# Performance work log

Measured on AMD Instinct MI355X. Metric: run time of the kernel, lower is better.

Reference implementation:

```python
import jax, jax.numpy as jnp
import numpy as np

N_STEPS = 10
LOG2PI = float(np.log(2.0 * np.pi))
# Dormand-Prince 5(4) tableau; only the 6 stages feeding the 5th-order solution (b7=0)
_C = (0.0, 1/5, 3/10, 4/5, 8/9, 1.0)
_A = ((),
      (1/5,),
      (3/40, 9/40),
      (44/45, -56/15, 32/9),
      (19372/6561, -25360/2187, 64448/6561, -212/729),
      (9017/3168, -355/33, 46732/5247, 49/176, -5103/18656))
_B = (35/384, 0.0, 500/1113, 125/192, -2187/6784, 11/84)


def _mlp(x, t, cond, W1, b1, W2, b2, W3, b3):
    # state_time_derivative_fn: f(t, x; cond) -> dx/dt
    tcol = jnp.full((x.shape[0], 1), t, dtype=x.dtype)
    h = jnp.concatenate([x, tcol, cond], axis=-1)
    h = jnp.tanh(h @ W1 + b1)
    h = jnp.tanh(h @ W2 + b2)
    return h @ W3 + b3


def _flow_log_prob(x, cond, eps, params):
    """FFJORD log_prob: integrate augmented state (x, logdet) from t=1 -> t=0
    with fixed-step DOPRI5; Hutchinson trace eps^T J eps via jvp."""
    B, D = x.shape

    def dyn(xx, t):
        f = lambda u: _mlp(u, t, cond, *params)
        dx, jeps = jax.jvp(f, (xx,), (eps,))
        tr = jnp.sum(jeps * eps, axis=-1)  # [B] Hutchinson trace estimate
        return dx, tr

    dt = -1.0 / N_STEPS  # integrate backward in time (inverse / log_prob pass)

    def step(carry, t0):
        xx, L = carry
        kx, kl = [], []
        for i in range(6):
            xi = xx
            for j in range(i):
                xi = xi + (dt * _A[i][j]) * kx[j]
            dxi, tri = dyn(xi, t0 + _C[i] * dt)
            kx.append(dxi)
            kl.append(tri)
        xx = xx + dt * sum(b * k for b, k in zip(_B, kx))
        L = L + dt * sum(b * k for b, k in zip(_B, kl))
        return (xx, L), None

    ts = 1.0 + dt * jnp.arange(N_STEPS, dtype=x.dtype)
    (z, L), _ = jax.lax.scan(jax.checkpoint(step), (x, jnp.zeros(B, x.dtype)), ts)
    # base distribution: standard multivariate normal
    logpz = -0.5 * jnp.sum(z * z, axis=-1) - 0.5 * D * LOG2PI
    return logpz + L


def setup_inputs() -> dict:
    key = jax.random.key(0)
    B, D, E, C, H = 8192, 504, 45, 1, 512
    ks = jax.random.split(key, 20)
    g = lambda k, shp: jax.random.normal(k, shp, jnp.float32)
    w = lambda k, fi, fo: g(k, (fi, fo)) * (1.0 / np.sqrt(fi))
    inp = {
        'voxel': g(ks[0], (B, D)),
        'energy': g(ks[1], (B, E)),
        'cond': jax.random.uniform(ks[2], (B, C), jnp.float32),
        'eps_v': g(ks[3], (B, D)),
        'eps_e': g(ks[4], (B, E)),
        # voxel-flow MLP: input = [x(D), t(1), energy(E)+cond(C)]
        'W1v': w(ks[5], D + 1 + E + C, H), 'b1v': jnp.zeros((H,), jnp.float32),
        'W2v': w(ks[6], H, H), 'b2v': jnp.zeros((H,), jnp.float32),
        'W3v': w(ks[7], H, D) * 0.1, 'b3v': jnp.zeros((D,), jnp.float32),
        # energy-flow MLP: input = [e(E), t(1), cond(C)]
        'W1e': w(ks[8], E + 1 + C, H), 'b1e': jnp.zeros((H,), jnp.float32),
        'W2e': w(ks[9], H, H), 'b2e': jnp.zeros((H,), jnp.float32),
        'W3e': w(ks[10], H, E) * 0.1, 'b3e': jnp.zeros((E,), jnp.float32),
    }
    return inp


def reference(voxel, energy, cond, eps_v, eps_e,
              W1v, b1v, W2v, b2v, W3v, b3v,
              W1e, b1e, W2e, b2e, W3e, b3e):
    # log_loss: voxel flow conditioned on concat([energies, conditional])
    cond_v = jnp.concatenate([energy, cond], axis=-1)
    lp_v = _flow_log_prob(voxel, cond_v, eps_v, (W1v, b1v, W2v, b2v, W3v, b3v))
    # log_loss_energy: energy flow conditioned on conditional
    lp_e = _flow_log_prob(energy, cond, eps_e, (W1e, b1e, W2e, b2e, W3e, b3e))
    loss_voxel = -jnp.mean(lp_v)
    loss_energy = -jnp.mean(lp_e)
    return loss_voxel + loss_energy
```

## Files before the change

### kernel.cpp

```cpp
#include <hip/hip_runtime.h>
#include <math.h>
#include <stdint.h>

#define LOG2PI 1.8378770664093453f

typedef __attribute__((ext_vector_type(8))) short bf8;
typedef __attribute__((ext_vector_type(4))) float f4;

__device__ __forceinline__ short f2bf(float f) {
    uint32_t u = __float_as_uint(f);
    u += 0x7fffu + ((u >> 16) & 1u);
    return (short)(u >> 16);
}
__device__ __forceinline__ float bf2f(unsigned short u) {
    return __uint_as_float(((uint32_t)u) << 16);
}
__device__ __forceinline__ float tanh_fast(float x) {
    float t = __builtin_amdgcn_exp2f(x * 2.88539008177793f);
    return 1.f - 2.f * __builtin_amdgcn_rcpf(1.f + t);
}
__device__ __forceinline__ bf8 ntl8(const short* p) {
    return *(const bf8*)p;
}
__device__ __forceinline__ void gload16(const void* g, void* l) {
    __builtin_amdgcn_global_load_lds(
        (const __attribute__((address_space(1))) uint32_t*)(uintptr_t)g,
        (__attribute__((address_space(3))) uint32_t*)(uintptr_t)l, 16, 0, 0);
}

struct FA {
    float* Pcurf; short* Pcurb; const short* th1b; const short* vbufp;
    short* Pk; float* xf;
    const short* w2t; const short* w3c;
    const float* b2; const float* b3p; const float* b31; const float* wtp;
    float* L;
};

__global__ __launch_bounds__(512, 2) void stage2_k(
    FA f0, FA f1, int i, float ti,
    float c0, float c1, float c2, float c3, float c4,
    float tcoef, float db0, float db2, float db3, float db4, float db5)
{
    __shared__ char lds[65536];
    const int tid = threadIdx.x, wave = tid >> 6, lane = tid & 63;
    const int lr = lane >> 4, lc = lane & 15;
    const int fl = blockIdx.x >> 8;
    const int bi = blockIdx.x & 255;
    const int m0 = bi * 32;
    const FA F = fl ? f1 : f0;
    const int dpad = fl ? 64 : 512;
    const bool doTan = (i != 1);
    const size_t BH = (size_t)8192 * 512;
    const float cj[5] = {c0, c1, c2, c3, c4};

    #pragma unroll
    for (int g = 0; g < 4; ++g) {
        int flat = (g << 12) + (tid << 3);
        int row = flat >> 9;
        int cc  = flat & 511;
        size_t gb = (((size_t)(m0 + row)) << 9) + cc;
        bf8 pcb = ntl8(F.Pcurb + gb);
        float4 w0 = *(const float4*)(F.wtp + cc);
        float4 w1 = *(const float4*)(F.wtp + cc + 4);
        float wv[8] = {w0.x,w0.y,w0.z,w0.w,w1.x,w1.y,w1.z,w1.w};
        float pre[8];
        #pragma unroll
        for (int e = 0; e < 8; ++e)
            pre[e] = fmaf(ti, wv[e], bf2f((unsigned short)pcb[e]));
        #pragma unroll
        for (int j = 0; j < 5; ++j) {
            if (j < i) {
                bf8 v = ntl8(F.Pk + (size_t)j * BH + gb);
                #pragma unroll
                for (int e = 0; e < 8; ++e)
                    pre[e] = fmaf(cj[j], bf2f((unsigned short)v[e]), pre[e]);
            }
        }
        int wb = (row << 10) + ((cc << 1) ^ ((row & 7) << 4));
        bf8 o1, o2;
        if (doTan) {
            bf8 th = ntl8(F.th1b + gb);
            #pragma unroll
            for (int e = 0; e < 8; ++e) {
                float a = tanh_fast(pre[e]);
                o1[e] = f2bf(a);
                o2[e] = f2bf((1.f - a * a) * bf2f((unsigned short)th[e]));
            }
            *(bf8*)(lds + wb) = o1;
            *(bf8*)(lds + 32768 + wb) = o2;
        } else {
            #pragma unroll
            for (int e = 0; e < 8; ++e) o1[e] = f2bf(tanh_fast(pre[e]));
            *(bf8*)(lds + wb) = o1;
        }
    }
    __syncthreads();

    f4 acc[4][4];
    #pragma unroll
    for (int mt = 0; mt < 4; ++mt)
        #pragma unroll
        for (int nt = 0; nt < 4; ++nt) acc[mt][nt] = (f4)0.0f;
    {
        const short* wb = F.w2t + ((size_t)((wave << 6) + lc) << 9) + (lr << 3);
        bf8 bc[4], bn[4];
        #pragma unroll
        for (int nt = 0; nt < 4; ++nt) bc[nt] = *(const bf8*)(wb + (nt << 13));
        for (int kt = 0; kt < 16; ++kt) {
            bf8 af[4];
            int kb = (kt << 6) + (lr << 4);
            #pragma unroll
            for (int mt = 0; mt < 4; ++mt) {
                if (mt >= 2 && !doTan) continue;
                int lrow = (mt << 4) + lc;
                af[mt] = *(const bf8*)(lds + (lrow << 10) + (kb ^ ((lrow & 7) << 4)));
            }
            if (kt < 15) {
                #pragma unroll
                for (int nt = 0; nt < 4; ++nt)
                    bn[nt] = *(const bf8*)(wb + (nt << 13) + ((kt + 1) << 5));
            }
            #pragma unroll
            for (int mt = 0; mt < 4; ++mt) {
                if (mt >= 2 && !doTan) continue;
                #pragma unroll
                for (int nt = 0; nt < 4; ++nt)
                    acc[mt][nt] = __builtin_amdgcn_mfma_f32_16x16x32_bf16(
                        af[mt], bc[nt], acc[mt][nt], 0, 0, 0);
            }
            #pragma unroll
            for (int nt = 0; nt < 4; ++nt) bc[nt] = bn[nt];
        }
    }
    __syncthreads();

    {
        bf8 vb[4];
        if (doTan) {
            size_t vbase = ((size_t)((bi << 9) + tid)) << 5;
            #pragma unroll
            for (int q = 0; q < 4; ++q) vb[q] = ntl8(F.vbufp + vbase + (q << 3));
        }
        float trp[2][4] = {{0.f,0.f,0.f,0.f},{0.f,0.f,0.f,0.f}};
        #pragma unroll
        for (int mt = 0; mt < 2; ++mt)
            #pragma unroll
            for (int nt = 0; nt < 4; ++nt) {
                int col = (wave << 6) + (nt << 4) + lc;
                float bb = F.b2[col];
                #pragma unroll
                for (int r = 0; r < 4; ++r) {
                    int lrow = (mt << 4) + (lr << 2) + r;
                    float a = tanh_fast(acc[mt][nt][r] + bb);
                    *(short*)(lds + (lrow << 10) + ((col << 1) ^ ((lrow & 7) << 4))) = f2bf(a);
                    if (doTan) {
                        int e = nt * 8 + mt * 4 + r;
                        float ta2 = (1.f - a * a) * acc[mt + 2][nt][r];
                        trp[mt][r] = fmaf(ta2,
                            bf2f((unsigned short)vb[e >> 3][e & 7]), trp[mt][r]);
                    }
                }
            }
        if (doTan) {
            #pragma unroll
            for (int mt = 0; mt < 2; ++mt)
                #pragma unroll
                for (int r = 0; r < 4; ++r) {
                    float v = trp[mt][r];
                    v += __shfl_xor(v, 1); v += __shfl_xor(v, 2);
                    v += __shfl_xor(v, 4); v += __shfl_xor(v, 8);
                    if (lc == 0)
                        atomicAdd(&F.L[m0 + (mt << 4) + (lr << 2) + r], tcoef * v);
                }
        }
    }
    __syncthreads();

    if (doTan) {
        if (fl == 0) {
            f4 aA[2][4];
            #pragma unroll
            for (int mt = 0; mt < 2; ++mt)
                #pragma unroll
                for (int nt = 0; nt < 4; ++nt) aA[mt][nt] = (f4)0.0f;
            const short* wA = F.w3c + ((size_t)((wave << 6) + lc) << 9) + (lr << 3);
            bf8 bc[4], bn[4];
            #pragma unroll
            for (int nt = 0; nt < 4; ++nt) bc[nt] = *(const bf8*)(wA + (nt << 13));
            for (int kt = 0; kt < 16; ++kt) {
                bf8 af[2];
                int kb = (kt << 6) + (lr << 4);
                #pragma unroll
                for (int mt = 0; mt < 2; ++mt) {
                    int lrow = (mt << 4) + lc;
                    af[mt] = *(const bf8*)(lds + (lrow << 10) + (kb ^ ((lrow & 7) << 4)));
                }
                if (kt < 15) {
                    #pragma unroll
                    for (int nt = 0; nt < 4; ++nt)
                        bn[nt] = *(const bf8*)(wA + (nt << 13) + ((kt + 1) << 5));
                }
                #pragma unroll
                for (int mt = 0; mt < 2; ++mt)
                    #pragma unroll
                    for (int nt = 0; nt < 4; ++nt)
                        aA[mt][nt] = __builtin_amdgcn_mfma_f32_16x16x32_bf16(
                            af[mt], bc[nt], aA[mt][nt], 0, 0, 0);
                #pragma unroll
                for (int nt = 0; nt < 4; ++nt) bc[nt] = bn[nt];
            }
            #pragma unroll
            for (int mt = 0; mt < 2; ++mt)
                #pragma unroll
                for (int nt = 0; nt < 4; ++nt) {
                    int col = (wave << 6) + (nt << 4) + lc;
                    float bb = F.b3p[col];
                    #pragma unroll
                    for (int r = 0; r < 4; ++r) {
                        size_t grow = (size_t)(m0 + (mt << 4) + (lr << 2) + r);
                        size_t xi = (grow << 9) + col;
                        F.xf[xi] = fmaf(tcoef, aA[mt][nt][r] + bb, F.xf[xi]);
                    }
                }
        } else if (wave < 4) {
            f4 aA[2];
            aA[0] = (f4)0.0f; aA[1] = (f4)0.0f;
            int col = (wave << 4) + lc;
            const short* wA = F.w3c + ((size_t)col << 9) + (lr << 3);
            bf8 bc = *(const bf8*)wA, bn;
            for (int kt = 0; kt < 16; ++kt) {
                bf8 af[2];
                int kb = (kt << 6) + (lr << 4);
                #pragma unroll
                for (int mt = 0; mt < 2; ++mt) {
                    int lrow = (mt << 4) + lc;
                    af[mt] = *(const bf8*)(lds + (lrow << 10) + (kb ^ ((lrow & 7) << 4)));
                }
                if (kt < 15) bn = *(const bf8*)(wA + ((kt + 1) << 5));
                #pragma unroll
                for (int mt = 0; mt < 2; ++mt)
                    aA[mt] = __builtin_amdgcn_mfma_f32_16x16x32_bf16(
                        af[mt], bc, aA[mt], 0, 0, 0);
                bc = bn;
            }
            float bb = F.b3p[col];
            #pragma unroll
            for (int mt = 0; mt < 2; ++mt)
                #pragma unroll
                for (int r = 0; r < 4; ++r) {
                    size_t grow = (size_t)(m0 + (mt << 4) + (lr << 2) + r);
                    size_t xi = (grow << 6) + col;
                    F.xf[xi] = fmaf(tcoef, aA[mt][r] + bb, F.xf[xi]);
                }
        }
    }

    {
        f4 aB[2][4];
        #pragma unroll
        for (int mt = 0; mt < 2; ++mt)
            #pragma unroll
            for (int nt = 0; nt < 4; ++nt) aB[mt][nt] = (f4)0.0f;
        const short* wB = F.w3c + ((size_t)(dpad + (wave << 6) + lc) << 9) + (lr << 3);
        bf8 bc[4], bn[4];
        #pragma unroll
        for (int nt = 0; nt < 4; ++nt) bc[nt] = *(const bf8*)(wB + (nt << 13));
        for (int kt = 0; kt < 16; ++kt) {
            bf8 af[2];
            int kb = (kt << 6) + (lr << 4);
            #pragma unroll
            for (int mt = 0; mt < 2; ++mt) {
                int lrow = (mt << 4) + lc;
                af[mt] = *(const bf8*)(lds + (lrow << 10) + (kb ^ ((lrow & 7) << 4)));
            }
            if (kt < 15) {
                #pragma unroll
                for (int nt = 0; nt < 4; ++nt)
                    bn[nt] = *(const bf8*)(wB + (nt << 13) + ((kt + 1) << 5));
            }
            #pragma unroll
            for (int mt = 0; mt < 2; ++mt)
                #pragma unroll
                for (int nt = 0; nt < 4; ++nt)
                    aB[mt][nt] = __builtin_amdgcn_mfma_f32_16x16x32_bf16(
                        af[mt], bc[nt], aB[mt][nt], 0, 0, 0);
            #pragma unroll
            for (int nt = 0; nt < 4; ++nt) bc[nt] = bn[nt];
        }
        #pragma unroll
        for (int mt = 0; mt < 2; ++mt)
            #pragma unroll
            for (int nt = 0; nt < 4; ++nt) {
                int colh = (wave << 6) + (nt << 4) + lc;
                float bb = F.b31[colh];
                #pragma unroll
                for (int r = 0; r < 4; ++r) {
                    int lrow = (mt << 4) + (lr << 2) + r;
                    *(short*)(lds + 32768 + (lrow << 10) +
                        ((colh << 1) ^ ((lrow & 7) << 4))) = f2bf(aB[mt][nt][r] + bb);
                }
            }
    }
    __syncthreads();

    #pragma unroll
    for (int g = 0; g < 4; ++g) {
        int flat = (g << 12) + (tid << 3);
        int row = flat >> 9;
        int cc  = flat & 511;
        size_t gb = (((size_t)(m0 + row)) << 9) + cc;
        bf8 pv = *(const bf8*)(lds + 32768 + (row << 10) +
                               ((cc << 1) ^ ((row & 7) << 4)));
        if (i < 5) {
            *(bf8*)(F.Pk + (size_t)i * BH + gb) = pv;
        } else {
            bf8 v0 = ntl8(F.Pk + 0 * BH + gb);
            bf8 v2 = ntl8(F.Pk + 2 * BH + gb);
            bf8 v3 = ntl8(F.Pk + 3 * BH + gb);
            bf8 v4 = ntl8(F.Pk + 4 * BH + gb);
            float4 pf0 = *(const float4*)(F.Pcurf + gb);
            float4 pf1 = *(const float4*)(F.Pcurf + gb + 4);
            float pf[8] = {pf0.x,pf0.y,pf0.z,pf0.w,pf1.x,pf1.y,pf1.z,pf1.w};
            bf8 ob;
            #pragma unroll
            for (int e = 0; e < 8; ++e) {
                float pn = pf[e];
                pn = fmaf(db0, bf2f((unsigned short)v0[e]), pn);
                pn = fmaf(db2, bf2f((unsigned short)v2[e]), pn);
                pn = fmaf(db3, bf2f((unsigned short)v3[e]), pn);
                pn = fmaf(db4, bf2f((unsigned short)v4[e]), pn);
                pn = fmaf(db5, bf2f((unsigned short)pv[e]), pn);
                pf[e] = pn;
                ob[e] = f2bf(pn);
            }
            *(float4*)(F.Pcurf + gb)     = make_float4(pf[0], pf[1], pf[2], pf[3]);
            *(float4*)(F.Pcurf + gb + 4) = make_float4(pf[4], pf[5], pf[6], pf[7]);
            *(bf8*)(F.Pcurb + gb) = ob;
        }
    }
}

template<int OUT>
__global__ __launch_bounds__(256) void mgemm0(
    const short* __restrict__ A, const short* __restrict__ Bt, int K,
    float* __restrict__ Cf, short* __restrict__ Cb,
    const float* __restrict__ bias)
{
    __shared__ char lds[32768];
    const int tid = threadIdx.x, wave = tid >> 6, lane = tid & 63;
    const int m0 = blockIdx.y * 128, n0 = blockIdx.x * 128;
    const int wr = wave >> 1, wc = wave & 1;

    f4 acc[4][4];
    #pragma unroll
    for (int m = 0; m < 4; ++m)
        #pragma unroll
        for (int n = 0; n < 4; ++n) acc[m][n] = (f4)0.0f;

    const int cbs  = (((lane & 7) ^ (lane >> 3)) << 4);
    const int lrow = lane >> 3;

    for (int k0 = 0; k0 < K; k0 += 64) {
        __syncthreads();
        #pragma unroll
        for (int i = 0; i < 4; ++i) {
            int q = wave * 4 + i;
            int row = q * 8 + lrow;
            gload16((const char*)(A  + (size_t)(m0 + row) * K + k0) + cbs, lds + q * 1024);
            gload16((const char*)(Bt + (size_t)(n0 + row) * K + k0) + cbs, lds + 16384 + q * 1024);
        }
        __syncthreads();
        #pragma unroll
        for (int kk = 0; kk < 2; ++kk) {
            bf8 af[4], bfr[4];
            #pragma unroll
            for (int m = 0; m < 4; ++m) {
                int row = wr * 64 + m * 16 + (lane & 15);
                int cb  = (((lane >> 4) << 4) + (kk << 6)) ^ ((row & 7) << 4);
                af[m] = *(const bf8*)(lds + row * 128 + cb);
            }
            #pragma unroll
            for (int n = 0; n < 4; ++n) {
                int row = wc * 64 + n * 16 + (lane & 15);
                int cb  = (((lane >> 4) << 4) + (kk << 6)) ^ ((row & 7) << 4);
                bfr[n] = *(const bf8*)(lds + 16384 + row * 128 + cb);
            }
            #pragma unroll
            for (int m = 0; m < 4; ++m)
                #pragma unroll
                for (int n = 0; n < 4; ++n)
                    acc[m][n] = __builtin_amdgcn_mfma_f32_16x16x32_bf16(
                        af[m], bfr[n], acc[m][n], 0, 0, 0);
        }
    }

    #pragma unroll
    for (int m = 0; m < 4; ++m)
        #pragma unroll
        for (int r = 0; r < 4; ++r) {
            int grow = m0 + wr * 64 + m * 16 + (lane >> 4) * 4 + r;
            #pragma unroll
            for (int n = 0; n < 4; ++n) {
                int gcol = n0 + wc * 64 + n * 16 + (lane & 15);
                float v = acc[m][n][r];
                if (bias) v += bias[gcol];
                if constexpr (OUT == 0) Cf[(size_t)grow * 512 + gcol] = v;
                else if constexpr (OUT == 1) Cb[(size_t)grow * 512 + gcol] = f2bf(v);
                else {
                    Cf[(size_t)grow * 512 + gcol] = v;
                    Cb[(size_t)grow * 512 + gcol] = f2bf(v);
                }
            }
        }
}

__global__ __launch_bounds__(256) void buildw1x(
    short* __restrict__ out, const float* __restrict__ W1,
    int D, int Dpad, int Kext, int extN, int rowE, int rowC, int total)
{
    int i = blockIdx.x * 256 + threadIdx.x;
    if (i >= total) return;
    int n = i / Kext, k = i - n * Kext;
    float v = 0.f;
    if (k < D) v = W1[(size_t)k * 512 + n];
    else if (k >= Dpad) {
        int j = k - Dpad;
        if (j < extN)       v = W1[(size_t)(rowE + j) * 512 + n];
        else if (j == extN) v = W1[(size_t)rowC * 512 + n];
    }
    out[i] = f2bf(v);
}

__global__ __launch_bounds__(256) void buildab(
    short* __restrict__ out, const float* __restrict__ x,
    const float* __restrict__ e, const float* __restrict__ c,
    int D, int Dpad, int Kext, int extN, int total)
{
    int i = blockIdx.x * 256 + threadIdx.x;
    if (i >= total) return;
    int b = i / Kext, k = i - b * Kext;
    float v = 0.f;
    if (k < D) v = x[(size_t)b * D + k];
    else if (k >= Dpad) {
        int j = k - Dpad;
        if (e && j < extN)       v = e[(size_t)b * 45 + j];
        else if (c && j == extN) v = c[b];
    }
    out[i] = f2bf(v);
}

__global__ __launch_bounds__(256) void padbf(
    short* __restrict__ out, const float* __restrict__ in,
    int K, int Kpad, int total)
{
    int i = blockIdx.x * 256 + threadIdx.x;
    if (i >= total) return;
    int n = i / Kpad, k = i - n * Kpad;
    out[i] = (k < K) ? f2bf(in[(size_t)n * K + k]) : (short)0;
}

__global__ __launch_bounds__(256) void convtrans(
    short* __restrict__ out, const float* __restrict__ in,
    int K, int N, int Kpad, int total)
{
    int i = blockIdx.x * 256 + threadIdx.x;
    if (i >= total) return;
    int n = i / Kpad, k = i - n * Kpad;
    out[i] = (k < K && n < N) ? f2bf(in[(size_t)k * N + n]) : (short)0;
}

__global__ __launch_bounds__(256) void padx(
    float* __restrict__ out, const float* __restrict__ in,
    int D, int Dpad, int total)
{
    int i = blockIdx.x * 256 + threadIdx.x;
    if (i >= total) return;
    int b = i / Dpad, d = i - b * Dpad;
    out[i] = (d < D) ? in[(size_t)b * D + d] : 0.f;
}

__global__ __launch_bounds__(256) void padvec(
    float* __restrict__ out, const float* __restrict__ in, int N, int Npad)
{
    int i = blockIdx.x * 256 + threadIdx.x;
    if (i < Npad) out[i] = (i < N) ? in[i] : 0.f;
}

__global__ __launch_bounds__(256) void b31k(
    float* __restrict__ b31, const float* __restrict__ b3,
    const float* __restrict__ W1, int D)
{
    __shared__ float ps[4];
    int n = blockIdx.x;
    int lane = threadIdx.x & 63, wave = threadIdx.x >> 6;
    float s = 0.f;
    for (int d = threadIdx.x; d < D; d += 256)
        s = fmaf(b3[d], W1[(size_t)d * 512 + n], s);
    #pragma unroll
    for (int off = 32; off; off >>= 1) s += __shfl_down(s, off, 64);
    if (lane == 0) ps[wave] = s;
    __syncthreads();
    if (threadIdx.x == 0) b31[n] = ps[0] + ps[1] + ps[2] + ps[3];
}

__global__ __launch_bounds__(512) void permvb(
    short* __restrict__ out, const short* __restrict__ in)
{
    int bi = blockIdx.x, tid = threadIdx.x;
    int wave = tid >> 6, lane = tid & 63, lr = lane >> 4, lc = lane & 15;
    int m0 = bi * 32;
    size_t obase = ((size_t)((bi << 9) + tid)) << 5;
    #pragma unroll
    for (int q = 0; q < 4; ++q) {
        bf8 o;
        #pragma unroll
        for (int k = 0; k < 8; ++k) {
            int e = q * 8 + k;
            int nt = e >> 3, mt = (e >> 2) & 1, r = e & 3;
            int row = m0 + mt * 16 + lr * 4 + r;
            int col = (wave << 6) + (nt << 4) + lc;
            o[k] = in[((size_t)row << 9) + col];
        }
        *(bf8*)(out + obase + (q << 3)) = o;
    }
}

__global__ __launch_bounds__(256) void final_reduce(
    const float* __restrict__ z, const float* __restrict__ L,
    float* __restrict__ acc, int Dpad, int Dtrue)
{
    __shared__ float ps[4];
    int wave = threadIdx.x >> 6, lane = threadIdx.x & 63;
    int row = blockIdx.x * 4 + wave;
    const float* zp = z + (size_t)row * Dpad;
    float s = 0.f;
    for (int d = lane; d < Dpad; d += 64) { float x = zp[d]; s = fmaf(x, x, s); }
    #pragma unroll
    for (int off = 32; off; off >>= 1) s += __shfl_down(s, off, 64);
    if (lane == 0) ps[wave] = -0.5f * s - 0.5f * (float)Dtrue * LOG2PI + L[row];
    __syncthreads();
    if (threadIdx.x == 0) atomicAdd(acc, ps[0] + ps[1] + ps[2] + ps[3]);
}

__global__ void finalize_k(float* __restrict__ out, const float* __restrict__ acc)
{
    out[0] = -(acc[0] + acc[1]) * (1.f / 8192.f);
}

extern "C" void kernel_launch(void* const* d_in, const int* in_sizes, int n_in,
                              void* d_out, int out_size, void* d_ws, size_t ws_size,
                              hipStream_t stream)
{
    (void)in_sizes; (void)n_in; (void)out_size; (void)ws_size;
    const float* voxel  = (const float*)d_in[0];
    const float* energy = (const float*)d_in[1];
    const float* cond   = (const float*)d_in[2];
    const float* eps_v  = (const float*)d_in[3];
    const float* eps_e  = (const float*)d_in[4];
    const float* Wt[2][5] = {
        {(const float*)d_in[5], (const float*)d_in[6], (const float*)d_in[7], (const float*)d_in[8], (const float*)d_in[9]},
        {(const float*)d_in[11],(const float*)d_in[12],(const float*)d_in[13],(const float*)d_in[14],(const float*)d_in[15]}};
    const float* b3t[2] = {(const float*)d_in[10], (const float*)d_in[16]};

    const int Bn = 8192, H = 512;
    const size_t BH = (size_t)Bn * H;

    char* wp = (char*)d_ws;
    auto alloc = [&](size_t bytes) { char* p = wp; wp += (bytes + 255) & ~(size_t)255; return p; };
    FA fa[2];
    for (int f = 0; f < 2; ++f) {
        fa[f].Pcurf = (float*)alloc(BH * 4);
        fa[f].Pcurb = (short*)alloc(BH * 2);
        fa[f].th1b  = (short*)alloc(BH * 2);
        fa[f].vbufp = (short*)alloc(BH * 2);
        fa[f].Pk    = (short*)alloc(5 * BH * 2);
        fa[f].xf    = (float*)alloc((size_t)Bn * (f ? 64 : 512) * 4);
        fa[f].w2t   = (short*)alloc((size_t)512 * 512 * 2);
        fa[f].w3c   = (short*)alloc((size_t)(f ? 576 : 1024) * 512 * 2);
        fa[f].b3p   = (float*)alloc(512 * 4);
        fa[f].b31   = (float*)alloc(512 * 4);
        fa[f].L     = (float*)alloc(Bn * 4);
    }
    short* abx   = (short*)alloc((size_t)Bn * 576 * 2);
    short* abeps = (short*)alloc((size_t)Bn * 576 * 2);
    short* vbtmp = (short*)alloc(BH * 2);
    short* w1x   = (short*)alloc((size_t)512 * 576 * 2);
    short* w3bt  = (short*)alloc((size_t)512 * 576 * 2);
    float* w31f  = (float*)alloc((size_t)512 * 512 * 4);
    float* acc   = (float*)alloc(256);

    (void)hipMemsetAsync(acc, 0, 2 * sizeof(float), stream);

    static const double AD[6][5] = {
        {0,0,0,0,0},
        {1.0/5,0,0,0,0},
        {3.0/40,9.0/40,0,0,0},
        {44.0/45,-56.0/15,32.0/9,0,0},
        {19372.0/6561,-25360.0/2187,64448.0/6561,-212.0/729,0},
        {9017.0/3168,-355.0/33,46732.0/5247,49.0/176,-5103.0/18656}};
    static const double Bcf[6] = {35.0/384, 0.0, 500.0/1113, 125.0/192, -2187.0/6784, 11.0/84};
    static const double CD[6]  = {0.0, 0.2, 0.3, 0.8, 8.0/9.0, 1.0};
    const double dtd = -0.1;

    for (int flow = 0; flow < 2; ++flow) {
        const int D    = (flow == 0) ? 504 : 45;
        const int Dpad = (flow == 0) ? 512 : 64;
        const int Kext = Dpad + 64;
        const int extN = (flow == 0) ? 45 : 0;
        const int rowE = (flow == 0) ? 505 : 0;
        const int rowC = (flow == 0) ? 550 : 46;
        const float* x_in = (flow == 0) ? voxel : energy;
        const float* eps  = (flow == 0) ? eps_v : eps_e;
        const float* ecnd = (flow == 0) ? energy : nullptr;
        const float* W1 = Wt[flow][0]; const float* b1 = Wt[flow][1];
        const float* W2 = Wt[flow][2]; const float* b2 = Wt[flow][3];
        const float* W3 = Wt[flow][4]; const float* b3 = b3t[flow];
        fa[flow].b2  = b2;
        fa[flow].wtp = W1 + (size_t)D * H;

        (void)hipMemsetAsync(fa[flow].L, 0, Bn * sizeof(float), stream);

        buildw1x<<<(512 * Kext + 255) / 256, 256, 0, stream>>>(
            w1x, W1, D, Dpad, Kext, extN, rowE, rowC, 512 * Kext);
        buildab<<<(Bn * Kext + 255) / 256, 256, 0, stream>>>(
            abx, x_in, ecnd, cond, D, Dpad, Kext, extN, Bn * Kext);
        buildab<<<(Bn * Kext + 255) / 256, 256, 0, stream>>>(
            abeps, eps, nullptr, nullptr, D, Dpad, Kext, extN, Bn * Kext);
        padbf<<<(512 * Kext + 255) / 256, 256, 0, stream>>>(w3bt, W3, D, Kext, 512 * Kext);
        convtrans<<<(512 * 512 + 255) / 256, 256, 0, stream>>>(
            (short*)fa[flow].w2t, W2, 512, 512, 512, 512 * 512);
        mgemm0<0><<<dim3(4, 4), 256, 0, stream>>>(w3bt, w1x, Kext, w31f, nullptr, nullptr);
        convtrans<<<(Dpad * 512 + 255) / 256, 256, 0, stream>>>(
            (short*)fa[flow].w3c, W3, 512, D, 512, Dpad * 512);
        convtrans<<<(512 * 512 + 255) / 256, 256, 0, stream>>>(
            (short*)fa[flow].w3c + (size_t)Dpad * 512, w31f, 512, 512, 512, 512 * 512);
        b31k<<<512, 256, 0, stream>>>((float*)fa[flow].b31, b3, W1, D);
        padvec<<<2, 256, 0, stream>>>((float*)fa[flow].b3p, b3, D, Dpad);
        padx<<<(Bn * Dpad + 255) / 256, 256, 0, stream>>>(fa[flow].xf, x_in, D, Dpad, Bn * Dpad);

        mgemm0<2><<<dim3(4, 64), 256, 0, stream>>>(abx, w1x, Kext,
            fa[flow].Pcurf, fa[flow].Pcurb, b1);
        mgemm0<1><<<dim3(4, 64), 256, 0, stream>>>(abeps, w1x, Kext,
            nullptr, (short*)fa[flow].th1b, nullptr);
        mgemm0<1><<<dim3(4, 64), 256, 0, stream>>>(abeps, w3bt, Kext,
            nullptr, vbtmp, nullptr);
        permvb<<<256, 512, 0, stream>>>((short*)fa[flow].vbufp, vbtmp);
    }

    const float db0 = (float)(dtd * Bcf[0]), db2 = (float)(dtd * Bcf[2]),
                db3 = (float)(dtd * Bcf[3]), db4 = (float)(dtd * Bcf[4]),
                db5 = (float)(dtd * Bcf[5]);

    for (int s = 0; s < 10; ++s) {
        float t0f = 1.0f + (float)s * -0.1f;
        for (int i = 0; i < 6; ++i) {
            float ti = t0f + (float)(CD[i] * dtd);
            float c[5] = {0,0,0,0,0};
            for (int j = 0; j < i; ++j) c[j] = (float)(dtd * AD[i][j]);
            float tc = (float)(dtd * Bcf[i]);
            stage2_k<<<512, 512, 0, stream>>>(fa[0], fa[1], i, ti,
                c[0], c[1], c[2], c[3], c[4], tc, db0, db2, db3, db4, db5);
        }
    }

    final_reduce<<<Bn / 4, 256, 0, stream>>>(fa[0].xf, fa[0].L, acc + 0, 512, 504);
    final_reduce<<<Bn / 4, 256, 0, stream>>>(fa[1].xf, fa[1].L, acc + 1, 64, 45);
    finalize_k<<<1, 1, 0, stream>>>((float*)d_out, acc);
}
```

Before: 6.506 ms.

## Merge sixty per-stage launches into one persistent kernel looping over RK stages

Replaces the 60 stage2_k launches (10 steps × 6 DOPRI5 stages) with a single persistent kernel. Each block loops over all stages internally and reads the tableau coefficients from constant memory. This works because each block only touches its own 32 rows, so no grid-wide barrier is needed between stages. It removes per-launch overhead and inter-kernel gaps, at the cost of recomputing coefficients on the device and possibly different register allocation from the runtime stage index.

```diff
diff --git a/kernel.cpp b/kernel.cpp
--- a/kernel.cpp
+++ b/kernel.cpp
@@ -6,6 +6,17 @@
 
 typedef __attribute__((ext_vector_type(8))) short bf8;
 typedef __attribute__((ext_vector_type(4))) float f4;
+
+__device__ __constant__ float ADc[6][5] = {
+    {0.f,0.f,0.f,0.f,0.f},
+    {0.2f,0.f,0.f,0.f,0.f},
+    {0.075f,0.225f,0.f,0.f,0.f},
+    {0.9777777778f,-3.7333333333f,3.5555555556f,0.f,0.f},
+    {2.9525986893f,-11.5957933340f,9.8228928855f,-0.2908093278f,0.f},
+    {2.8462752526f,-10.7575757576f,8.9064227177f,0.2784090909f,-0.2735313036f}};
+__device__ __constant__ float CDc[6] = {0.f,0.2f,0.3f,0.8f,0.8888888889f,1.f};
+__device__ __constant__ float Bcc[6] = {0.0911458333f,0.f,0.4492362983f,
+    0.6510416667f,-0.3223761792f,0.1309523810f};
 
 __device__ __forceinline__ short f2bf(float f) {
     uint32_t u = __float_as_uint(f);
@@ -36,10 +47,9 @@
     float* L;
 };
 
-__global__ __launch_bounds__(512, 2) void stage2_k(
-    FA f0, FA f1, int i, float ti,
-    float c0, float c1, float c2, float c3, float c4,
-    float tcoef, float db0, float db2, float db3, float db4, float db5)
+__global__ __launch_bounds__(512, 2) void persist2_k(
+    FA f0, FA f1,
+    float db0, float db2, float db3, float db4, float db5)
 {
     __shared__ char lds[65536];
     const int tid = threadIdx.x, wave = tid >> 6, lane = tid & 63;
@@ -49,144 +59,230 @@
     const int m0 = bi * 32;
     const FA F = fl ? f1 : f0;
     const int dpad = fl ? 64 : 512;
-    const bool doTan = (i != 1);
     const size_t BH = (size_t)8192 * 512;
-    const float cj[5] = {c0, c1, c2, c3, c4};
-
-    #pragma unroll
-    for (int g = 0; g < 4; ++g) {
-        int flat = (g << 12) + (tid << 3);
-        int row = flat >> 9;
-        int cc  = flat & 511;
-        size_t gb = (((size_t)(m0 + row)) << 9) + cc;
-        bf8 pcb = ntl8(F.Pcurb + gb);
-        float4 w0 = *(const float4*)(F.wtp + cc);
-        float4 w1 = *(const float4*)(F.wtp + cc + 4);
-        float wv[8] = {w0.x,w0.y,w0.z,w0.w,w1.x,w1.y,w1.z,w1.w};
-        float pre[8];
-        #pragma unroll
-        for (int e = 0; e < 8; ++e)
-            pre[e] = fmaf(ti, wv[e], bf2f((unsigned short)pcb[e]));
-        #pragma unroll
-        for (int j = 0; j < 5; ++j) {
-            if (j < i) {
-                bf8 v = ntl8(F.Pk + (size_t)j * BH + gb);
-                #pragma unroll
-                for (int e = 0; e < 8; ++e)
-                    pre[e] = fmaf(cj[j], bf2f((unsigned short)v[e]), pre[e]);
-            }
-        }
-        int wb = (row << 10) + ((cc << 1) ^ ((row & 7) << 4));
-        bf8 o1, o2;
+
+    #pragma unroll 1
+    for (int st = 0; st < 60; ++st) {
+        const int s = st / 6, i = st - s * 6;
+        const float ti = 1.f - 0.1f * (float)s - 0.1f * CDc[i];
+        const float tcoef = -0.1f * Bcc[i];
+        const bool doTan = (i != 1);
+        float cj[5];
+        #pragma unroll
+        for (int j = 0; j < 5; ++j) cj[j] = -0.1f * ADc[i][j];
+
+        #pragma unroll
+        for (int g = 0; g < 4; ++g) {
+            int flat = (g << 12) + (tid << 3);
+            int row = flat >> 9;
+            int cc  = flat & 511;
+            size_t gb = (((size_t)(m0 + row)) << 9) + cc;
+            bf8 pcb = ntl8(F.Pcurb + gb);
+            float4 w0 = *(const float4*)(F.wtp + cc);
+            float4 w1 = *(const float4*)(F.wtp + cc + 4);
+            float wv[8] = {w0.x,w0.y,w0.z,w0.w,w1.x,w1.y,w1.z,w1.w};
+            float pre[8];
+            #pragma unroll
+            for (int e = 0; e < 8; ++e)
+                pre[e] = fmaf(ti, wv[e], bf2f((unsigned short)pcb[e]));
+            #pragma unroll
+            for (int j = 0; j < 5; ++j) {
+                if (j < i) {
+                    bf8 v = ntl8(F.Pk + (size_t)j * BH + gb);
+                    #pragma unroll
+                    for (int e = 0; e < 8; ++e)
+                        pre[e] = fmaf(cj[j], bf2f((unsigned short)v[e]), pre[e]);
+                }
+            }
+            int wb = (row << 10) + ((cc << 1) ^ ((row & 7) << 4));
+            bf8 o1, o2;
+            if (doTan) {
+                bf8 th = ntl8(F.th1b + gb);
+                #pragma unroll
+                for (int e = 0; e < 8; ++e) {
+                    float a = tanh_fast(pre[e]);
+                    o1[e] = f2bf(a);
+                    o2[e] = f2bf((1.f - a * a) * bf2f((unsigned short)th[e]));
+                }
+                *(bf8*)(lds + wb) = o1;
+                *(bf8*)(lds + 32768 + wb) = o2;
+            } else {
+                #pragma unroll
+                for (int e = 0; e < 8; ++e) o1[e] = f2bf(tanh_fast(pre[e]));
+                *(bf8*)(lds + wb) = o1;
+            }
+        }
+        __syncthreads();
+
+        f4 acc[4][4];
+        #pragma unroll
+        for (int mt = 0; mt < 4; ++mt)
+            #pragma unroll
+            for (int nt = 0; nt < 4; ++nt) acc[mt][nt] = (f4)0.0f;
+        {
+            const short* wb = F.w2t + ((size_t)((wave << 6) + lc) << 9) + (lr << 3);
+            bf8 bc[4], bn[4];
+            #pragma unroll
+            for (int nt = 0; nt < 4; ++nt) bc[nt] = *(const bf8*)(wb + (nt << 13));
+            for (int kt = 0; kt < 16; ++kt) {
+                bf8 af[4];
+                int kb = (kt << 6) + (lr << 4);
+                #pragma unroll
+                for (int mt = 0; mt < 4; ++mt) {
+                    if (mt >= 2 && !doTan) continue;
+                    int lrow = (mt << 4) + lc;
+                    af[mt] = *(const bf8*)(lds + (lrow << 10) + (kb ^ ((lrow & 7) << 4)));
+                }
+                if (kt < 15) {
+                    #pragma unroll
+                    for (int nt = 0; nt < 4; ++nt)
+                        bn[nt] = *(const bf8*)(wb + (nt << 13) + ((kt + 1) << 5));
+                }
+                #pragma unroll
+                for (int mt = 0; mt < 4; ++mt) {
+                    if (mt >= 2 && !doTan) continue;
+                    #pragma unroll
+                    for (int nt = 0; nt < 4; ++nt)
+                        acc[mt][nt] = __builtin_amdgcn_mfma_f32_16x16x32_bf16(
+                            af[mt], bc[nt], acc[mt][nt], 0, 0, 0);
+                }
+                #pragma unroll
+                for (int nt = 0; nt < 4; ++nt) bc[nt] = bn[nt];
+            }
+        }
+        __syncthreads();
+
+        {
+            bf8 vb[4];
+            if (doTan) {
+                size_t vbase = ((size_t)((bi << 9) + tid)) << 5;
+                #pragma unroll
+                for (int q = 0; q < 4; ++q) vb[q] = ntl8(F.vbufp + vbase + (q << 3));
+            }
+            float trp[2][4] = {{0.f,0.f,0.f,0.f},{0.f,0.f,0.f,0.f}};
+            #pragma unroll
+            for (int mt = 0; mt < 2; ++mt)
+                #pragma unroll
+                for (int nt = 0; nt < 4; ++nt) {
+                    int col = (wave << 6) + (nt << 4) + lc;
+                    float bb = F.b2[col];
+                    #pragma unroll
+                    for (int r = 0; r < 4; ++r) {
+                        int lrow = (mt << 4) + (lr << 2) + r;
+                        float a = tanh_fast(acc[mt][nt][r] + bb);
+                        *(short*)(lds + (lrow << 10) + ((col << 1) ^ ((lrow & 7) << 4))) = f2bf(a);
+                        if (doTan) {
+                            int e = nt * 8 + mt * 4 + r;
+                            float ta2 = (1.f - a * a) * acc[mt + 2][nt][r];
+                            trp[mt][r] = fmaf(ta2,
+                                bf2f((unsigned short)vb[e >> 3][e & 7]), trp[mt][r]);
+                        }
+                    }
+                }
+            if (doTan) {
+                #pragma unroll
+                for (int mt = 0; mt < 2; ++mt)
+                    #pragma unroll
+                    for (int r = 0; r < 4; ++r) {
+                        float v = trp[mt][r];
+                        v += __shfl_xor(v, 1); v += __shfl_xor(v, 2);
+                        v += __shfl_xor(v, 4); v += __shfl_xor(v, 8);
+                        if (lc == 0)
+                            atomicAdd(&F.L[m0 + (mt << 4) + (lr << 2) + r], tcoef * v);
+                    }
+            }
+        }
+        __syncthreads();
+
         if (doTan) {
-            bf8 th = ntl8(F.th1b + gb);
-            #pragma unroll
-            for (int e = 0; e < 8; ++e) {
-                float a = tanh_fast(pre[e]);
-                o1[e] = f2bf(a);
-                o2[e] = f2bf((1.f - a * a) * bf2f((unsigned short)th[e]));
-            }
-            *(bf8*)(lds + wb) = o1;
-            *(bf8*)(lds + 32768 + wb) = o2;
-        } else {
-            #pragma unroll
-            for (int e = 0; e < 8; ++e) o1[e] = f2bf(tanh_fast(pre[e]));
-            *(bf8*)(lds + wb) = o1;
-        }
-    }
-    __syncthreads();
-
-    f4 acc[4][4];
-    #pragma unroll
-    for (int mt = 0; mt < 4; ++mt)
-        #pragma unroll
-        for (int nt = 0; nt < 4; ++nt) acc[mt][nt] = (f4)0.0f;
-    {
-        const short* wb = F.w2t + ((size_t)((wave << 6) + lc) << 9) + (lr << 3);
-        bf8 bc[4], bn[4];
-        #pragma unroll
-        for (int nt = 0; nt < 4; ++nt) bc[nt] = *(const bf8*)(wb + (nt << 13));
-        for (int kt = 0; kt < 16; ++kt) {
-            bf8 af[4];
-            int kb = (kt << 6) + (lr << 4);
-            #pragma unroll
-            for (int mt = 0; mt < 4; ++mt) {
-                if (mt >= 2 && !doTan) continue;
-                int lrow = (mt << 4) + lc;
-                af[mt] = *(const bf8*)(lds + (lrow << 10) + (kb ^ ((lrow & 7) << 4)));
-            }
-            if (kt < 15) {
-                #pragma unroll
-                for (int nt = 0; nt < 4; ++nt)
-                    bn[nt] = *(const bf8*)(wb + (nt << 13) + ((kt + 1) << 5));
-            }
-            #pragma unroll
-            for (int mt = 0; mt < 4; ++mt) {
-                if (mt >= 2 && !doTan) continue;
-                #pragma unroll
-                for (int nt = 0; nt < 4; ++nt)
-                    acc[mt][nt] = __builtin_amdgcn_mfma_f32_16x16x32_bf16(
-                        af[mt], bc[nt], acc[mt][nt], 0, 0, 0);
-            }
-            #pragma unroll
-            for (int nt = 0; nt < 4; ++nt) bc[nt] = bn[nt];
-        }
-    }
-    __syncthreads();
-
-    {
-        bf8 vb[4];
-        if (doTan) {
-            size_t vbase = ((size_t)((bi << 9) + tid)) << 5;
-            #pragma unroll
-            for (int q = 0; q < 4; ++q) vb[q] = ntl8(F.vbufp + vbase + (q << 3));
-        }
-        float trp[2][4] = {{0.f,0.f,0.f,0.f},{0.f,0.f,0.f,0.f}};
-        #pragma unroll
-        for (int mt = 0; mt < 2; ++mt)
-            #pragma unroll
-            for (int nt = 0; nt < 4; ++nt) {
-                int col = (wave << 6) + (nt << 4) + lc;
-                float bb = F.b2[col];
-                #pragma unroll
-                for (int r = 0; r < 4; ++r) {
-                    int lrow = (mt << 4) + (lr << 2) + r;
-                    float a = tanh_fast(acc[mt][nt][r] + bb);
-                    *(short*)(lds + (lrow << 10) + ((col << 1) ^ ((lrow & 7) << 4))) = f2bf(a);
-                    if (doTan) {
-                        int e = nt * 8 + mt * 4 + r;
-                        float ta2 = (1.f - a * a) * acc[mt + 2][nt][r];
-                        trp[mt][r] = fmaf(ta2,
-                            bf2f((unsigned short)vb[e >> 3][e & 7]), trp[mt][r]);
-                    }
-                }
-            }
-        if (doTan) {
+            if (fl == 0) {
+                f4 aA[2][4];
+                #pragma unroll
+                for (int mt = 0; mt < 2; ++mt)
+                    #pragma unroll
+                    for (int nt = 0; nt < 4; ++nt) aA[mt][nt] = (f4)0.0f;
+                const short* wA = F.w3c + ((size_t)((wave << 6) + lc) << 9) + (lr << 3);
+                bf8 bc[4], bn[4];
+                #pragma unroll
+                for (int nt = 0; nt < 4; ++nt) bc[nt] = *(const bf8*)(wA + (nt << 13));
+                for (int kt = 0; kt < 16; ++kt) {
+                    bf8 af[2];
+                    int kb = (kt << 6) + (lr << 4);
+                    #pragma unroll
+                    for (int mt = 0; mt < 2; ++mt) {
+                        int lrow = (mt << 4) + lc;
+                        af[mt] = *(const bf8*)(lds + (lrow << 10) + (kb ^ ((lrow & 7) << 4)));
+                    }
+                    if (kt < 15) {
+                        #pragma unroll
+                        for (int nt = 0; nt < 4; ++nt)
+                            bn[nt] = *(const bf8*)(wA + (nt << 13) + ((kt + 1) << 5));
+                    }
+                    #pragma unroll
+                    for (int mt = 0; mt < 2; ++mt)
+                        #pragma unroll
+                        for (int nt = 0; nt < 4; ++nt)
+                            aA[mt][nt] = __builtin_amdgcn_mfma_f32_16x16x32_bf16(
+                                af[mt], bc[nt], aA[mt][nt], 0, 0, 0);
+                    #pragma unroll
+                    for (int nt = 0; nt < 4; ++nt) bc[nt] = bn[nt];
+                }
+                #pragma unroll
+                for (int mt = 0; mt < 2; ++mt)
+                    #pragma unroll
+                    for (int nt = 0; nt < 4; ++nt) {
+                        int col = (wave << 6) + (nt << 4) + lc;
+                        float bb = F.b3p[col];
+                        #pragma unroll
+                        for (int r = 0; r < 4; ++r) {
+                            size_t grow = (size_t)(m0 + (mt << 4) + (lr << 2) + r);
+                            size_t xi = (grow << 9) + col;
+                            F.xf[xi] = fmaf(tcoef, aA[mt][nt][r] + bb, F.xf[xi]);
+                        }
+                    }
+            } else if (wave < 4) {
+                f4 aA[2];
+                aA[0] = (f4)0.0f; aA[1] = (f4)0.0f;
+                int col = (wave << 4) + lc;
+                const short* wA = F.w3c + ((size_t)col << 9) + (lr << 3);
+                bf8 bc = *(const bf8*)wA, bn;
+                for (int kt = 0; kt < 16; ++kt) {
+                    bf8 af[2];
+                    int kb = (kt << 6) + (lr << 4);
+                    #pragma unroll
+                    for (int mt = 0; mt < 2; ++mt) {
+                        int lrow = (mt << 4) + lc;
+                        af[mt] = *(const bf8*)(lds + (lrow << 10) + (kb ^ ((lrow & 7) << 4)));
+                    }
+                    if (kt < 15) bn = *(const bf8*)(wA + ((kt + 1) << 5));
+                    #pragma unroll
+                    for (int mt = 0; mt < 2; ++mt)
+                        aA[mt] = __builtin_amdgcn_mfma_f32_16x16x32_bf16(
+                            af[mt], bc, aA[mt], 0, 0, 0);
+                    bc = bn;
+                }
+                float bb = F.b3p[col];
+                #pragma unroll
+                for (int mt = 0; mt < 2; ++mt)
+                    #pragma unroll
+                    for (int r = 0; r < 4; ++r) {
+                        size_t grow = (size_t)(m0 + (mt << 4) + (lr << 2) + r);
+                        size_t xi = (grow << 6) + col;
+                        F.xf[xi] = fmaf(tcoef, aA[mt][r] + bb, F.xf[xi]);
+                    }
+            }
+        }
+
+        {
+            f4 aB[2][4];
             #pragma unroll
             for (int mt = 0; mt < 2; ++mt)
                 #pragma unroll
-                for (int r = 0; r < 4; ++r) {
-                    float v = trp[mt][r];
-                    v += __shfl_xor(v, 1); v += __shfl_xor(v, 2);
-                    v += __shfl_xor(v, 4); v += __shfl_xor(v, 8);
-                    if (lc == 0)
-                        atomicAdd(&F.L[m0 + (mt << 4) + (lr << 2) + r], tcoef * v);
-                }
-        }
-    }
-    __syncthreads();
-
-    if (doTan) {
-        if (fl == 0) {
-            f4 aA[2][4];
-            #pragma unroll
-            for (int mt = 0; mt < 2; ++mt)
-                #pragma unroll
-                for (int nt = 0; nt < 4; ++nt) aA[mt][nt] = (f4)0.0f;
-            const short* wA = F.w3c + ((size_t)((wave << 6) + lc) << 9) + (lr << 3);
+                for (int nt = 0; nt < 4; ++nt) aB[mt][nt] = (f4)0.0f;
+            const short* wB = F.w3c + ((size_t)(dpad + (wave << 6) + lc) << 9) + (lr << 3);
             bf8 bc[4], bn[4];
             #pragma unroll
-            for (int nt = 0; nt < 4; ++nt) bc[nt] = *(const bf8*)(wA + (nt << 13));
+            for (int nt = 0; nt < 4; ++nt) bc[nt] = *(const bf8*)(wB + (nt << 13));
             for (int kt = 0; kt < 16; ++kt) {
                 bf8 af[2];
                 int kb = (kt << 6) + (lr << 4);
@@ -198,14 +294,14 @@
                 if (kt < 15) {
                     #pragma unroll
                     for (int nt = 0; nt < 4; ++nt)
-                        bn[nt] = *(const bf8*)(wA + (nt << 13) + ((kt + 1) << 5));
+                        bn[nt] = *(const bf8*)(wB + (nt << 13) + ((kt + 1) << 5));
                 }
                 #pragma unroll
                 for (int mt = 0; mt < 2; ++mt)
                     #pragma unroll
                     for (int nt = 0; nt < 4; ++nt)
-                        aA[mt][nt] = __builtin_amdgcn_mfma_f32_16x16x32_bf16(
-                            af[mt], bc[nt], aA[mt][nt], 0, 0, 0);
+                        aB[mt][nt] = __builtin_amdgcn_mfma_f32_16x16x32_bf16(
+                            af[mt], bc[nt], aB[mt][nt], 0, 0, 0);
                 #pragma unroll
                 for (int nt = 0; nt < 4; ++nt) bc[nt] = bn[nt];
             }
@@ -213,130 +309,54 @@
             for (int mt = 0; mt < 2; ++mt)
                 #pragma unroll
                 for (int nt = 0; nt < 4; ++nt) {
-                    int col = (wave << 6) + (nt << 4) + lc;
-                    float bb = F.b3p[col];
+                    int colh = (wave << 6) + (nt << 4) + lc;
+                    float bb = F.b31[colh];
                     #pragma unroll
                     for (int r = 0; r < 4; ++r) {
-                        size_t grow = (size_t)(m0 + (mt << 4) + (lr << 2) + r);
-                        size_t xi = (grow << 9) + col;
-                        F.xf[xi] = fmaf(tcoef, aA[mt][nt][r] + bb, F.xf[xi]);
-                    }
-                }
-        } else if (wave < 4) {
-            f4 aA[2];
-            aA[0] = (f4)0.0f; aA[1] = (f4)0.0f;
-            int col = (wave << 4) + lc;
-            const short* wA = F.w3c + ((size_t)col << 9) + (lr << 3);
-            bf8 bc = *(const bf8*)wA, bn;
-            for (int kt = 0; kt < 16; ++kt) {
-                bf8 af[2];
-                int kb = (kt << 6) + (lr << 4);
-                #pragma unroll
-                for (int mt = 0; mt < 2; ++mt) {
-                    int lrow = (mt << 4) + lc;
-                    af[mt] = *(const bf8*)(lds + (lrow << 10) + (kb ^ ((lrow & 7) << 4)));
-                }
-                if (kt < 15) bn = *(const bf8*)(wA + ((kt + 1) << 5));
-                #pragma unroll
-                for (int mt = 0; mt < 2; ++mt)
-                    aA[mt] = __builtin_amdgcn_mfma_f32_16x16x32_bf16(
-                        af[mt], bc, aA[mt], 0, 0, 0);
-                bc = bn;
-            }
-            float bb = F.b3p[col];
-            #pragma unroll
-            for (int mt = 0; mt < 2; ++mt)
-                #pragma unroll
-                for (int r = 0; r < 4; ++r) {
-                    size_t grow = (size_t)(m0 + (mt << 4) + (lr << 2) + r);
-                    size_t xi = (grow << 6) + col;
-                    F.xf[xi] = fmaf(tcoef, aA[mt][r] + bb, F.xf[xi]);
-                }
-        }
-    }
-
-    {
-        f4 aB[2][4];
-        #pragma unroll
-        for (int mt = 0; mt < 2; ++mt)
-            #pragma unroll
-            for (int nt = 0; nt < 4; ++nt) aB[mt][nt] = (f4)0.0f;
-        const short* wB = F.w3c + ((size_t)(dpad + (wave << 6) + lc) << 9) + (lr << 3);
-        bf8 bc[4], bn[4];
-        #pragma unroll
-        for (int nt = 0; nt < 4; ++nt) bc[nt] = *(const bf8*)(wB + (nt << 13));
-        for (int kt = 0; kt < 16; ++kt) {
-            bf8 af[2];
-            int kb = (kt << 6) + (lr << 4);
-            #pragma unroll
-            for (int mt = 0; mt < 2; ++mt) {
-                int lrow = (mt << 4) + lc;
-                af[mt] = *(const bf8*)(lds + (lrow << 10) + (kb ^ ((lrow & 7) << 4)));
-            }
-            if (kt < 15) {
-                #pragma unroll
-                for (int nt = 0; nt < 4; ++nt)
-                    bn[nt] = *(const bf8*)(wB + (nt << 13) + ((kt + 1) << 5));
-            }
-            #pragma unroll
-            for (int mt = 0; mt < 2; ++mt)
-                #pragma unroll
-                for (int nt = 0; nt < 4; ++nt)
-                    aB[mt][nt] = __builtin_amdgcn_mfma_f32_16x16x32_bf16(
-                        af[mt], bc[nt], aB[mt][nt], 0, 0, 0);
-            #pragma unroll
-            for (int nt = 0; nt < 4; ++nt) bc[nt] = bn[nt];
-        }
-        #pragma unroll
-        for (int mt = 0; mt < 2; ++mt)
-            #pragma unroll
-            for (int nt = 0; nt < 4; ++nt) {
-                int colh = (wave << 6) + (nt << 4) + lc;
-                float bb = F.b31[colh];
-                #pragma unroll
-                for (int r = 0; r < 4; ++r) {
-                    int lrow = (mt << 4) + (lr << 2) + r;
-                    *(short*)(lds + 32768 + (lrow << 10) +
-                        ((colh << 1) ^ ((lrow & 7) << 4))) = f2bf(aB[mt][nt][r] + bb);
-                }
-            }
-    }
-    __syncthreads();
-
-    #pragma unroll
-    for (int g = 0; g < 4; ++g) {
-        int flat = (g << 12) + (tid << 3);
-        int row = flat >> 9;
-        int cc  = flat & 511;
-        size_t gb = (((size_t)(m0 + row)) << 9) + cc;
-        bf8 pv = *(const bf8*)(lds + 32768 + (row << 10) +
-                               ((cc << 1) ^ ((row & 7) << 4)));
-        if (i < 5) {
-            *(bf8*)(F.Pk + (size_t)i * BH + gb) = pv;
-        } else {
-            bf8 v0 = ntl8(F.Pk + 0 * BH + gb);
-            bf8 v2 = ntl8(F.Pk + 2 * BH + gb);
-            bf8 v3 = ntl8(F.Pk + 3 * BH + gb);
-            bf8 v4 = ntl8(F.Pk + 4 * BH + gb);
-            float4 pf0 = *(const float4*)(F.Pcurf + gb);
-            float4 pf1 = *(const float4*)(F.Pcurf + gb + 4);
-            float pf[8] = {pf0.x,pf0.y,pf0.z,pf0.w,pf1.x,pf1.y,pf1.z,pf1.w};
-            bf8 ob;
-            #pragma unroll
-            for (int e = 0; e < 8; ++e) {
-                float pn = pf[e];
-                pn = fmaf(db0, bf2f((unsigned short)v0[e]), pn);
-                pn = fmaf(db2, bf2f((unsigned short)v2[e]), pn);
-                pn = fmaf(db3, bf2f((unsigned short)v3[e]), pn);
-                pn = fmaf(db4, bf2f((unsigned short)v4[e]), pn);
-                pn = fmaf(db5, bf2f((unsigned short)pv[e]), pn);
-                pf[e] = pn;
-                ob[e] = f2bf(pn);
-            }
-            *(float4*)(F.Pcurf + gb)     = make_float4(pf[0], pf[1], pf[2], pf[3]);
-            *(float4*)(F.Pcurf + gb + 4) = make_float4(pf[4], pf[5], pf[6], pf[7]);
-            *(bf8*)(F.Pcurb + gb) = ob;
-        }
+                        int lrow = (mt << 4) + (lr << 2) + r;
+                        *(short*)(lds + 32768 + (lrow << 10) +
+                            ((colh << 1) ^ ((lrow & 7) << 4))) = f2bf(aB[mt][nt][r] + bb);
+                    }
+                }
+        }
+        __syncthreads();
+
+        #pragma unroll
+        for (int g = 0; g < 4; ++g) {
+            int flat = (g << 12) + (tid << 3);
+            int row = flat >> 9;
+            int cc  = flat & 511;
+            size_t gb = (((size_t)(m0 + row)) << 9) + cc;
+            bf8 pv = *(const bf8*)(lds + 32768 + (row << 10) +
+                                   ((cc << 1) ^ ((row & 7) << 4)));
+            if (i < 5) {
+                *(bf8*)(F.Pk + (size_t)i * BH + gb) = pv;
+            } else {
+                bf8 v0 = ntl8(F.Pk + 0 * BH + gb);
+                bf8 v2 = ntl8(F.Pk + 2 * BH + gb);
+                bf8 v3 = ntl8(F.Pk + 3 * BH + gb);
+                bf8 v4 = ntl8(F.Pk + 4 * BH + gb);
+                float4 pf0 = *(const float4*)(F.Pcurf + gb);
+                float4 pf1 = *(const float4*)(F.Pcurf + gb + 4);
+                float pf[8] = {pf0.x,pf0.y,pf0.z,pf0.w,pf1.x,pf1.y,pf1.z,pf1.w};
+                bf8 ob;
+                #pragma unroll
+                for (int e = 0; e < 8; ++e) {
+                    float pn = pf[e];
+                    pn = fmaf(db0, bf2f((unsigned short)v0[e]), pn);
+                    pn = fmaf(db2, bf2f((unsigned short)v2[e]), pn);
+                    pn = fmaf(db3, bf2f((unsigned short)v3[e]), pn);
+                    pn = fmaf(db4, bf2f((unsigned short)v4[e]), pn);
+                    pn = fmaf(db5, bf2f((unsigned short)pv[e]), pn);
+                    pf[e] = pn;
+                    ob[e] = f2bf(pn);
+                }
+                *(float4*)(F.Pcurf + gb)     = make_float4(pf[0], pf[1], pf[2], pf[3]);
+                *(float4*)(F.Pcurf + gb + 4) = make_float4(pf[4], pf[5], pf[6], pf[7]);
+                *(bf8*)(F.Pcurb + gb) = ob;
+            }
+        }
+        __syncthreads();
     }
 }
 
@@ -599,7 +619,6 @@
         {19372.0/6561,-25360.0/2187,64448.0/6561,-212.0/729,0},
         {9017.0/3168,-355.0/33,46732.0/5247,49.0/176,-5103.0/18656}};
     static const double Bcf[6] = {35.0/384, 0.0, 500.0/1113, 125.0/192, -2187.0/6784, 11.0/84};
-    static const double CD[6]  = {0.0, 0.2, 0.3, 0.8, 8.0/9.0, 1.0};
     const double dtd = -0.1;
 
     for (int flow = 0; flow < 2; ++flow) {
@@ -651,17 +670,7 @@
                 db3 = (float)(dtd * Bcf[3]), db4 = (float)(dtd * Bcf[4]),
                 db5 = (float)(dtd * Bcf[5]);
 
-    for (int s = 0; s < 10; ++s) {
-        float t0f = 1.0f + (float)s * -0.1f;
-        for (int i = 0; i < 6; ++i) {
-            float ti = t0f + (float)(CD[i] * dtd);
-            float c[5] = {0,0,0,0,0};
-            for (int j = 0; j < i; ++j) c[j] = (float)(dtd * AD[i][j]);
-            float tc = (float)(dtd * Bcf[i]);
-            stage2_k<<<512, 512, 0, stream>>>(fa[0], fa[1], i, ti,
-                c[0], c[1], c[2], c[3], c[4], tc, db0, db2, db3, db4, db5);
-        }
-    }
+    persist2_k<<<512, 512, 0, stream>>>(fa[0], fa[1], db0, db2, db3, db4, db5);
 
     final_reduce<<<Bn / 4, 256, 0, stream>>>(fa[0].xf, fa[0].L, acc + 0, 512, 504);
     final_reduce<<<Bn / 4, 256, 0, stream>>>(fa[1].xf, fa[1].L, acc + 1, 64, 45);
```

Result: slower. 10.90 ms (+67.6%).
